# Performance work log

Hardware: AMD Instinct MI355X
Metric: run time of the kernel (lower is better)

Reference implementation:

```python
import jax, jax.numpy as jnp
import numpy as np

DAMP_MIN = jnp.asarray([0.001, 0.001], dtype=jnp.float32)
B = 4194304


def setup_inputs() -> dict:
    key = jax.random.key(0)
    ks = jax.random.split(key, 14)
    rn = lambda k, s: jax.random.normal(k, s, dtype=jnp.float32)
    return {
        "x": rn(ks[0], (B, 2)),
        "w_d1": rn(ks[1], (2, 16)),
        "w_d2": rn(ks[2], (16, 16)),
        "w_d3": rn(ks[3], (16, 2)),
        "w_o1": rn(ks[4], (2, 16)),
        "w_o2": rn(ks[5], (16, 16)),
        "w_o3": rn(ks[6], (16, 1)),
        "b_d1": rn(ks[7], (16,)),
        "b_d2": rn(ks[8], (16,)),
        "b_d3": rn(ks[9], (2,)),
        "b_o1": rn(ks[10], (16,)),
        "b_o2": rn(ks[11], (16,)),
        "b_o3": rn(ks[12], (1,)),
    }


def reference(x, w_d1, w_d2, w_d3, w_o1, w_o2, w_o3,
              b_d1, b_d2, b_d3, b_o1, b_o2, b_o3) -> jnp.ndarray:
    # diag branch: 3-layer tanh MLP -> relu -> +damp_min -> * x   [B, 2]
    d = jnp.tanh(x @ w_d1 + b_d1)
    d = jnp.tanh(d @ w_d2 + b_d2)
    d3 = d @ w_d3 + b_d3
    d3r = (jax.nn.relu(d3) + DAMP_MIN) * x  # diag elements of L

    # off-diag branch: 3-layer tanh MLP -> scalar per sample   [B, 1]
    o = jnp.tanh(x @ w_o1 + b_o1)
    o = jnp.tanh(o @ w_o2 + b_o2)
    o3 = o @ w_o3 + b_o3

    # L = [[a, 0], [c, b]];  D_i = (L L^T) x_i, closed form for 2x2:
    # L L^T = [[a^2, a*c], [a*c, c^2 + b^2]]
    a = d3r[:, 0]
    b = d3r[:, 1]
    c = o3[:, 0]
    x0 = x[:, 0]
    x1 = x[:, 1]
    D0 = a * a * x0 + a * c * x1
    D1 = a * c * x0 + (c * c + b * b) * x1
    return jnp.stack([D0, D1], axis=1)  # [B, 2]
```

## Files before the change

### kernel.cpp

```cpp
#include <hip/hip_runtime.h>

#define BTOT 4194304
#define MPW 4

typedef __attribute__((ext_vector_type(4))) float f32x4;
typedef __attribute__((ext_vector_type(8))) short bf16x8;

#define KLOG 2.88539008177792681472f

__device__ __forceinline__ short f2bf(float f) {
  union { float f; unsigned u; } v; v.f = f;
  unsigned u = v.u;
  unsigned r = (u + 0x7FFFu + ((u >> 16) & 1u)) >> 16;
  return (short)r;
}
__device__ __forceinline__ float bf2f(short s) {
  union { unsigned u; float f; } v; v.u = ((unsigned)(unsigned short)s) << 16;
  return v.f;
}

__device__ __forceinline__ float tanh_pre(float y) {
  float t = __builtin_amdgcn_exp2f(y);
  float r = __builtin_amdgcn_rcpf(1.0f + t);
  return __builtin_fmaf(-2.0f, r, 1.0f);
}

__device__ __forceinline__ unsigned cvt_pk(float lo, float hi) {
  unsigned r;
  asm("v_cvt_pk_bf16_f32 %0, %1, %2" : "=v"(r) : "v"(lo), "v"(hi));
  return r;
}
__device__ __forceinline__ bf16x8 pack8(const float* h) {
  union { unsigned w[4]; bf16x8 v; } U;
  #pragma unroll
  for (int jw = 0; jw < 4; ++jw) U.w[jw] = cvt_pk(h[2 * jw], h[2 * jw + 1]);
  return U.v;
}

__global__ __launch_bounds__(256, 4)
void damping_kernel(const float* __restrict__ x,
                    const float* __restrict__ w_d1, const float* __restrict__ w_d2,
                    const float* __restrict__ w_d3, const float* __restrict__ w_o1,
                    const float* __restrict__ w_o2, const float* __restrict__ w_o3,
                    const float* __restrict__ b_d1, const float* __restrict__ b_d2,
                    const float* __restrict__ b_d3, const float* __restrict__ b_o1,
                    const float* __restrict__ b_o2, const float* __restrict__ b_o3,
                    float* __restrict__ out)
{
  const int tid  = blockIdx.x * blockDim.x + threadIdx.x;
  const int wave = tid >> 6;
  const int l    = threadIdx.x & 63;
  const int g    = l >> 4;
  const int c16  = l & 15;
  const int kbase = g * 8;

  float W0[8], W1[8], B1[8];
  #pragma unroll
  for (int j = 0; j < 8; ++j) {
    int f = kbase + j;
    if (f < 16) { W0[j] = KLOG * w_d1[f];      W1[j] = KLOG * w_d1[16 + f];      B1[j] = KLOG * b_d1[f]; }
    else        { W0[j] = KLOG * w_o1[f - 16]; W1[j] = KLOG * w_o1[16 + f - 16]; B1[j] = KLOG * b_o1[f - 16]; }
  }
  bf16x8 Adh, Adl, Aoh, Aol;
  #pragma unroll
  for (int j = 0; j < 8; ++j) {
    int k = kbase + j;
    float ad = (k < 16)  ? KLOG * w_d2[k * 16 + c16]        : 0.0f;
    float ao = (k >= 16) ? KLOG * w_o2[(k - 16) * 16 + c16] : 0.0f;
    short adh = f2bf(ad); Adh[j] = adh; Adl[j] = f2bf(ad - bf2f(adh));
    short aoh = f2bf(ao); Aoh[j] = aoh; Aol[j] = f2bf(ao - bf2f(aoh));
  }
  f32x4 Cd0, Co0;
  #pragma unroll
  for (int i = 0; i < 4; ++i) {
    int f = g * 4 + i;
    Cd0[i] = KLOG * b_d2[f]; Co0[i] = KLOG * b_o2[f];
  }

  const int rr = c16 & 3, tt = c16 >> 2;
  bf16x8 A3h[4];
  #pragma unroll
  for (int t = 0; t < 4; ++t) {
    #pragma unroll
    for (int j = 0; j < 8; ++j) {
      float val = 0.0f;
      if (t == tt) {
        if (rr == 0 && j < 4)  val = w_d3[(4 * g + j) * 2 + 0];
        if (rr == 1 && j < 4)  val = w_d3[(4 * g + j) * 2 + 1];
        if (rr == 2 && j >= 4) val = w_o3[4 * g + j - 4];
      }
      A3h[t][j] = f2bf(val);
    }
  }
  const float b30 = b_d3[0], b31 = b_d3[1], b3o = b_o3[0];

  const float2* x2 = (const float2*)x;

  for (int m = 0; m < MPW; ++m) {
    const int mbase = (wave * MPW + m) * 64;

    float2 xv4[4];
    #pragma unroll
    for (int t = 0; t < 4; ++t)
      xv4[t] = x2[mbase + t * 16 + c16];

    f32x4 acc3;
    acc3[0] = b30; acc3[1] = b31; acc3[2] = b3o; acc3[3] = 0.0f;

    #pragma unroll
    for (int t = 0; t < 4; ++t) {
      const float2 xv = xv4[t];

      float h[8];
      #pragma unroll
      for (int j = 0; j < 8; ++j)
        h[j] = tanh_pre(__builtin_fmaf(xv.y, W1[j], __builtin_fmaf(xv.x, W0[j], B1[j])));

      bf16x8 b1f = pack8(h);

      f32x4 accd = Cd0, acco = Co0;
      accd = __builtin_amdgcn_mfma_f32_16x16x32_bf16(Adh, b1f, accd, 0, 0, 0);
      accd = __builtin_amdgcn_mfma_f32_16x16x32_bf16(Adl, b1f, accd, 0, 0, 0);
      acco = __builtin_amdgcn_mfma_f32_16x16x32_bf16(Aoh, b1f, acco, 0, 0, 0);
      acco = __builtin_amdgcn_mfma_f32_16x16x32_bf16(Aol, b1f, acco, 0, 0, 0);

      float h2[8];
      #pragma unroll
      for (int i = 0; i < 4; ++i) {
        h2[i]     = tanh_pre(accd[i]);
        h2[4 + i] = tanh_pre(acco[i]);
      }
      bf16x8 b3f = pack8(h2);

      acc3 = __builtin_amdgcn_mfma_f32_16x16x32_bf16(A3h[t], b3f, acc3, 0, 0, 0);
    }

    const float2 xs = x2[mbase + l];
    float a = (fmaxf(acc3[0], 0.0f) + 0.001f) * xs.x;
    float b = (fmaxf(acc3[1], 0.0f) + 0.001f) * xs.y;
    float c = acc3[2];
    float D0 = a * __builtin_fmaf(a, xs.x, c * xs.y);
    float s  = __builtin_fmaf(c, c, b * b);
    float D1 = __builtin_fmaf(a * c, xs.x, s * xs.y);
    ((float2*)out)[mbase + l] = make_float2(D0, D1);
  }
}

extern "C" void kernel_launch(void* const* d_in, const int* in_sizes, int n_in,
                              void* d_out, int out_size, void* d_ws, size_t ws_size,
                              hipStream_t stream) {
  const float* x    = (const float*)d_in[0];
  const float* w_d1 = (const float*)d_in[1];
  const float* w_d2 = (const float*)d_in[2];
  const float* w_d3 = (const float*)d_in[3];
  const float* w_o1 = (const float*)d_in[4];
  const float* w_o2 = (const float*)d_in[5];
  const float* w_o3 = (const float*)d_in[6];
  const float* b_d1 = (const float*)d_in[7];
  const float* b_d2 = (const float*)d_in[8];
  const float* b_d3 = (const float*)d_in[9];
  const float* b_o1 = (const float*)d_in[10];
  const float* b_o2 = (const float*)d_in[11];
  const float* b_o3 = (const float*)d_in[12];
  float* out = (float*)d_out;

  const int waves  = BTOT / (64 * MPW);
  const int blocks = waves / 4;
  damping_kernel<<<blocks, 256, 0, stream>>>(x, w_d1, w_d2, w_d3, w_o1, w_o2, w_o3,
                                             b_d1, b_d2, b_d3, b_o1, b_o2, b_o3, out);
}
```

Before: 165.2 us.

## Replace hardware tanh with 64-entry cross-lane lookup table plus Taylor correction

Computes tanh through a 64-entry table held one value per lane and fetched with ds_bpermute. The nearest entry is refined with a second-order correction, and inputs are clamped to about ±4.6. This replaces the exp2 and reciprocal transcendental pair to cut transcendental-unit pressure. The tail x reload is also replaced by reusing values already in registers. Accuracy for saturated or large inputs depends on the clamp and table spacing, and the bpermute adds LDS-path traffic.

New measurement: 214.1 us. +29.6%, slower.

```diff
diff --git a/kernel.cpp b/kernel.cpp
--- a/kernel.cpp
+++ b/kernel.cpp
@@ -7,6 +7,9 @@
 typedef __attribute__((ext_vector_type(8))) short bf16x8;
 
 #define KLOG 2.88539008177792681472f
+#define TS   6.85f
+#define TINV (1.0f / TS)
+#define TOFFI 31.5f
 
 __device__ __forceinline__ short f2bf(float f) {
   union { float f; unsigned u; } v; v.f = f;
@@ -19,10 +22,23 @@
   return v.f;
 }
 
-__device__ __forceinline__ float tanh_pre(float y) {
-  float t = __builtin_amdgcn_exp2f(y);
+__device__ __forceinline__ float tanh_hw(float z) {
+  float t = __builtin_amdgcn_exp2f(KLOG * z);
   float r = __builtin_amdgcn_rcpf(1.0f + t);
   return __builtin_fmaf(-2.0f, r, 1.0f);
+}
+
+__device__ __forceinline__ float tanh_lut(float fi, int vtab_bits) {
+  fi = fminf(fmaxf(fi, 0.0f), 63.0f);
+  float fn = __builtin_rintf(fi);
+  float dz = (fi - fn) * TINV;
+  int   ii = (int)fn;
+  int   vb = __builtin_amdgcn_ds_bpermute(ii << 2, vtab_bits);
+  float v  = __builtin_bit_cast(float, vb);
+  float g  = __builtin_fmaf(-v, v, 1.0f);
+  float p  = dz * g;
+  float q  = __builtin_fmaf(-dz, v, 1.0f);
+  return __builtin_fmaf(p, q, v);
 }
 
 __device__ __forceinline__ unsigned cvt_pk(float lo, float hi) {
@@ -54,19 +70,22 @@
   const int c16  = l & 15;
   const int kbase = g * 8;
 
+  const float vtab = tanh_hw(((float)l - TOFFI) * TINV);
+  const int vtab_bits = __builtin_bit_cast(int, vtab);
+
   float W0[8], W1[8], B1[8];
   #pragma unroll
   for (int j = 0; j < 8; ++j) {
     int f = kbase + j;
-    if (f < 16) { W0[j] = KLOG * w_d1[f];      W1[j] = KLOG * w_d1[16 + f];      B1[j] = KLOG * b_d1[f]; }
-    else        { W0[j] = KLOG * w_o1[f - 16]; W1[j] = KLOG * w_o1[16 + f - 16]; B1[j] = KLOG * b_o1[f - 16]; }
+    if (f < 16) { W0[j] = TS * w_d1[f];      W1[j] = TS * w_d1[16 + f];      B1[j] = TS * b_d1[f] + TOFFI; }
+    else        { W0[j] = TS * w_o1[f - 16]; W1[j] = TS * w_o1[16 + f - 16]; B1[j] = TS * b_o1[f - 16] + TOFFI; }
   }
   bf16x8 Adh, Adl, Aoh, Aol;
   #pragma unroll
   for (int j = 0; j < 8; ++j) {
     int k = kbase + j;
-    float ad = (k < 16)  ? KLOG * w_d2[k * 16 + c16]        : 0.0f;
-    float ao = (k >= 16) ? KLOG * w_o2[(k - 16) * 16 + c16] : 0.0f;
+    float ad = (k < 16)  ? TS * w_d2[k * 16 + c16]        : 0.0f;
+    float ao = (k >= 16) ? TS * w_o2[(k - 16) * 16 + c16] : 0.0f;
     short adh = f2bf(ad); Adh[j] = adh; Adl[j] = f2bf(ad - bf2f(adh));
     short aoh = f2bf(ao); Aoh[j] = aoh; Aol[j] = f2bf(ao - bf2f(aoh));
   }
@@ -74,7 +93,7 @@
   #pragma unroll
   for (int i = 0; i < 4; ++i) {
     int f = g * 4 + i;
-    Cd0[i] = KLOG * b_d2[f]; Co0[i] = KLOG * b_o2[f];
+    Cd0[i] = TS * b_d2[f] + TOFFI; Co0[i] = TS * b_o2[f] + TOFFI;
   }
 
   const int rr = c16 & 3, tt = c16 >> 2;
@@ -114,7 +133,7 @@
       float h[8];
       #pragma unroll
       for (int j = 0; j < 8; ++j)
-        h[j] = tanh_pre(__builtin_fmaf(xv.y, W1[j], __builtin_fmaf(xv.x, W0[j], B1[j])));
+        h[j] = tanh_lut(__builtin_fmaf(xv.y, W1[j], __builtin_fmaf(xv.x, W0[j], B1[j])), vtab_bits);
 
       bf16x8 b1f = pack8(h);
 
@@ -127,15 +146,16 @@
       float h2[8];
       #pragma unroll
       for (int i = 0; i < 4; ++i) {
-        h2[i]     = tanh_pre(accd[i]);
-        h2[4 + i] = tanh_pre(acco[i]);
+        h2[i]     = tanh_lut(accd[i], vtab_bits);
+        h2[4 + i] = tanh_lut(acco[i], vtab_bits);
       }
       bf16x8 b3f = pack8(h2);
 
       acc3 = __builtin_amdgcn_mfma_f32_16x16x32_bf16(A3h[t], b3f, acc3, 0, 0, 0);
     }
 
-    const float2 xs = x2[mbase + l];
+    float2 xs = (g & 2) ? ((g & 1) ? xv4[3] : xv4[2])
+                        : ((g & 1) ? xv4[1] : xv4[0]);
     float a = (fmaxf(acc3[0], 0.0f) + 0.001f) * xs.x;
     float b = (fmaxf(acc3[1], 0.0f) + 0.001f) * xs.y;
     float c = acc3[2];
```
